# Performance work log

Measured on AMD Instinct MI355X. Metric: run time of the kernel, lower is better.

Reference implementation:

```python
import jax, jax.numpy as jnp
import numpy as np

N, E, C, Z, B, L = 50000, 800000, 32, 4, 8, 2
DEG = 16.0  # avg num neighbors = E / N


def ssp(x):
    # ShiftedSoftPlus
    return jax.nn.softplus(x) - jnp.log(2.0).astype(x.dtype)


def setup_inputs() -> dict:
    key = jax.random.key(0)
    ks = jax.random.split(key, 13)
    f32 = jnp.float32
    return {
        "node_features": jax.random.normal(ks[0], (N, 4 * C), f32),
        "node_attrs": jax.random.uniform(ks[1], (N, Z), f32),
        "edge_index": jax.random.randint(ks[2], (2, E), 0, N),
        "edge_embedding": jax.random.uniform(ks[3], (E, B), f32),
        "edge_attrs": jax.random.normal(ks[4], (E, 4), f32),
        "W0": jax.random.normal(ks[5], (L, C, C), f32) / np.sqrt(C),
        "W1": jax.random.normal(ks[6], (L, C, C), f32) / np.sqrt(C),
        "Wr1": jax.random.normal(ks[7], (L, B, B), f32) / np.sqrt(B),
        "Wr2": jax.random.normal(ks[8], (L, B, 5 * C), f32) / np.sqrt(B),
        "Ws": jax.random.normal(ks[9], (L, C, 2 * C), f32) / np.sqrt(C),
        "Wv": jax.random.normal(ks[10], (L, C, C), f32) / np.sqrt(C),
        "Wsc_s": jax.random.normal(ks[11], (L, C, Z, 2 * C), f32) / np.sqrt(C * Z),
        "Wsc_v": jax.random.normal(ks[12], (L, C, Z, C), f32) / np.sqrt(C * Z),
    }


def reference(node_features, node_attrs, edge_index, edge_embedding, edge_attrs,
              W0, W1, Wr1, Wr2, Ws, Wv, Wsc_s, Wsc_v):
    src, dst = edge_index[0], edge_index[1]
    Y0 = edge_attrs[:, :1]            # [E,1]  l=0 sph harmonic
    Yv = edge_attrs[:, 1:]            # [E,3]  l=1 sph harmonic
    x = node_features
    for l in range(L):
        s_in = x[:, :C]                          # [N,C]   scalars
        v_in = x[:, C:].reshape(N, C, 3)         # [N,C,3] vectors
        # linear (channel mixing per irrep)
        s = s_in @ W0[l]
        v = jnp.einsum('nci,cf->nfi', v_in, W1[l])
        # gather source node features per edge
        se = s[src]                              # [E,C]
        ve = v[src]                              # [E,C,3]
        # radial MLP -> per-edge tensor-product path weights (5 paths)
        w = jax.nn.silu(edge_embedding @ Wr1[l]) @ Wr2[l]   # [E,5C]
        w1, w2, w3, w4, w5 = jnp.split(w, 5, axis=-1)
        # tensor-product messages
        m_s = w1 * se * Y0 + w4 * jnp.einsum('eci,ei->ec', ve, Yv)          # 0ex0e->0e, 1ex1e->0e
        m_v = (w2[..., None] * se[..., None] * Yv[:, None, :]               # 0ex1e->1e
               + w3[..., None] * ve * Y0[..., None]                         # 1ex0e->1e
               + w5[..., None] * jnp.cross(ve, Yv[:, None, :]))             # 1ex1e->1e
        # scatter-sum to destination nodes, normalize by avg degree
        agg_s = jax.ops.segment_sum(m_s, dst, num_segments=N) / DEG
        agg_v = jax.ops.segment_sum(m_v, dst, num_segments=N) / DEG
        # output linear: scalars -> C feature scalars + C gates, vectors -> C
        out_s = agg_s @ Ws[l]                                               # [N,2C]
        out_v = jnp.einsum('nci,cf->nfi', agg_v, Wv[l])                     # [N,C,3]
        # self-connection (FullyConnectedTensorProduct with node_attrs)
        out_s = out_s + jnp.einsum('nc,nz,czf->nf', s_in, node_attrs, Wsc_s[l])
        out_v = out_v + jnp.einsum('nci,nz,czf->nfi', v_in, node_attrs, Wsc_v[l])
        # equivariant Gate nonlinearity
        feat = ssp(out_s[:, :C])
        gates = ssp(out_s[:, C:])
        gv = out_v * gates[..., None]
        new_x = jnp.concatenate([feat, gv.reshape(N, 3 * C)], axis=-1)
        x = x + new_x  # resnet (irreps match across layers)
    return x
```

## Files before the change

kernel.cpp:

```cpp
#include <hip/hip_runtime.h>
#include <math.h>

#define NN 50000
#define NE 800000
#define Cc 32
#define Zz 4
#define Bb 8
#define NL 2
#define DEG_INV (1.0f/16.0f)
#define SCAN_PAD 53248
#define EBLK (NE / 256)
#define NBLK (NN / 8)


__device__ __forceinline__ float ssp_f(float x) {
    float sp = fmaxf(x, 0.0f) + log1pf(expf(-fabsf(x)));
    return sp - 0.69314718055994530942f;
}
__device__ __forceinline__ float silu_f(float x) {
    return x / (1.0f + expf(-x));
}
__device__ __forceinline__ unsigned bf16rn(float f) {
    unsigned u = __float_as_uint(f);
    return (u + 0x7fffu + ((u >> 16) & 1u)) >> 16;
}


__global__ void hist_kernel(const int* __restrict__ ei, int* __restrict__ counts) {
    int e = blockIdx.x * 256 + threadIdx.x;
    if (e < NE) atomicAdd(&counts[ei[NE + e]], 1);
}

__global__ void scan_kernel(const int* __restrict__ counts,
                            int* __restrict__ base,
                            int* __restrict__ cursor) {
    __shared__ int partial[1024];
    int t = threadIdx.x;
    const int CH = 52;
    int b0 = t * CH;
    int sum = 0;
    #pragma unroll
    for (int i = 0; i < CH; i += 4) {
        int4 v = *(const int4*)(counts + b0 + i);
        sum += v.x + v.y + v.z + v.w;
    }
    partial[t] = sum;
    __syncthreads();
    for (int off = 1; off < 1024; off <<= 1) {
        int v = 0;
        if (t >= off) v = partial[t - off];
        __syncthreads();
        if (t >= off) partial[t] += v;
        __syncthreads();
    }
    int prefix = (t == 0) ? 0 : partial[t - 1];
    for (int i = b0; i < b0 + CH && i < NN; ++i) {
        base[i] = prefix;
        cursor[i] = prefix;
        prefix += counts[i];
    }
    if (t == 1023) base[NN] = partial[1023];
}

__global__ void prep_kernel(const int* __restrict__ ei,
                            const float* __restrict__ emb,
                            const float* __restrict__ eattr,
                            const float* __restrict__ Wr1,
                            int* __restrict__ cursor,
                            int* __restrict__ perm_src,
                            float* __restrict__ hS0,
                            float* __restrict__ hS1,
                            float* __restrict__ YS,
                            const float* __restrict__ nf,
                            const float* __restrict__ W0,
                            const float* __restrict__ W1,
                            float* __restrict__ x,
                            unsigned* __restrict__ svb) {
    __shared__ float wr1s[128];
    __shared__ float xs[8][128];
    int t = threadIdx.x;
    int b = blockIdx.x;
    if (b < EBLK) {
        if (t < 128) wr1s[t] = Wr1[t];
        __syncthreads();
        int e = b * 256 + t;
        int dst = ei[NE + e];
        int pos = atomicAdd(&cursor[dst], 1);
        perm_src[pos] = ei[e];

        const float4* s4 = (const float4*)emb + (size_t)e * 2;
        float4 a = s4[0], bb = s4[1];
        float em[8] = {a.x, a.y, a.z, a.w, bb.x, bb.y, bb.z, bb.w};
        float h0[8], h1[8];
        #pragma unroll
        for (int j = 0; j < 8; ++j) {
            float acc0 = 0.f, acc1 = 0.f;
            #pragma unroll
            for (int k = 0; k < 8; ++k) {
                acc0 = fmaf(em[k], wr1s[k * 8 + j], acc0);
                acc1 = fmaf(em[k], wr1s[64 + k * 8 + j], acc1);
            }
            h0[j] = silu_f(acc0);
            h1[j] = silu_f(acc1);
        }
        float4* o0 = (float4*)(hS0 + (size_t)pos * 8);
        o0[0] = make_float4(h0[0], h0[1], h0[2], h0[3]);
        o0[1] = make_float4(h0[4], h0[5], h0[6], h0[7]);
        float4* o1 = (float4*)(hS1 + (size_t)pos * 8);
        o1[0] = make_float4(h1[0], h1[1], h1[2], h1[3]);
        o1[1] = make_float4(h1[4], h1[5], h1[6], h1[7]);
        ((float4*)YS)[pos] = ((const float4*)eattr)[e];
    } else {
        int node0 = (b - EBLK) * 8;
        #pragma unroll
        for (int k = 0; k < 4; ++k) {
            int idx = t + k * 256;
            int n = idx >> 7, col = idx & 127;
            float val = nf[(size_t)(node0 + n) * 128 + col];
            xs[n][col] = val;
            x[(size_t)(node0 + n) * 128 + col] = val;
        }
        __syncthreads();
        int n = t >> 5, f = t & 31;
        int gn = node0 + n;
        float acc_s = 0.f, a0 = 0.f, a1 = 0.f, a2 = 0.f;
        #pragma unroll
        for (int c = 0; c < Cc; ++c) {
            float w0 = W0[c * Cc + f];
            float w1 = W1[c * Cc + f];
            acc_s = fmaf(xs[n][c], w0, acc_s);
            a0 = fmaf(xs[n][32 + c * 3 + 0], w1, a0);
            a1 = fmaf(xs[n][32 + c * 3 + 1], w1, a1);
            a2 = fmaf(xs[n][32 + c * 3 + 2], w1, a2);
        }
        unsigned* o = svb + (size_t)gn * 64;
        o[f]      = bf16rn(acc_s) | (bf16rn(a0) << 16);
        o[32 + f] = bf16rn(a1)    | (bf16rn(a2) << 16);
    }
}

#define PROC_EDGE(ha, hb, Yv, se, v0, v1, v2)                                \
    do {                                                                     \
        float hh0 = ha.x, hh1 = ha.y, hh2 = ha.z, hh3 = ha.w;                \
        float hh4 = hb.x, hh5 = hb.y, hh6 = hb.z, hh7 = hb.w;                \
        float w1 = 0.f, w2 = 0.f, w3 = 0.f, w4 = 0.f, w5 = 0.f;              \
        w1 = fmaf(hh0, wr2s[0][c], w1); w2 = fmaf(hh0, wr2s[0][32 + c], w2); \
        w3 = fmaf(hh0, wr2s[0][64 + c], w3); w4 = fmaf(hh0, wr2s[0][96 + c], w4); \
        w5 = fmaf(hh0, wr2s[0][128 + c], w5);                                \
        w1 = fmaf(hh1, wr2s[1][c], w1); w2 = fmaf(hh1, wr2s[1][32 + c], w2); \
        w3 = fmaf(hh1, wr2s[1][64 + c], w3); w4 = fmaf(hh1, wr2s[1][96 + c], w4); \
        w5 = fmaf(hh1, wr2s[1][128 + c], w5);                                \
        w1 = fmaf(hh2, wr2s[2][c], w1); w2 = fmaf(hh2, wr2s[2][32 + c], w2); \
        w3 = fmaf(hh2, wr2s[2][64 + c], w3); w4 = fmaf(hh2, wr2s[2][96 + c], w4); \
        w5 = fmaf(hh2, wr2s[2][128 + c], w5);                                \
        w1 = fmaf(hh3, wr2s[3][c], w1); w2 = fmaf(hh3, wr2s[3][32 + c], w2); \
        w3 = fmaf(hh3, wr2s[3][64 + c], w3); w4 = fmaf(hh3, wr2s[3][96 + c], w4); \
        w5 = fmaf(hh3, wr2s[3][128 + c], w5);                                \
        w1 = fmaf(hh4, wr2s[4][c], w1); w2 = fmaf(hh4, wr2s[4][32 + c], w2); \
        w3 = fmaf(hh4, wr2s[4][64 + c], w3); w4 = fmaf(hh4, wr2s[4][96 + c], w4); \
        w5 = fmaf(hh4, wr2s[4][128 + c], w5);                                \
        w1 = fmaf(hh5, wr2s[5][c], w1); w2 = fmaf(hh5, wr2s[5][32 + c], w2); \
        w3 = fmaf(hh5, wr2s[5][64 + c], w3); w4 = fmaf(hh5, wr2s[5][96 + c], w4); \
        w5 = fmaf(hh5, wr2s[5][128 + c], w5);                                \
        w1 = fmaf(hh6, wr2s[6][c], w1); w2 = fmaf(hh6, wr2s[6][32 + c], w2); \
        w3 = fmaf(hh6, wr2s[6][64 + c], w3); w4 = fmaf(hh6, wr2s[6][96 + c], w4); \
        w5 = fmaf(hh6, wr2s[6][128 + c], w5);                                \
        w1 = fmaf(hh7, wr2s[7][c], w1); w2 = fmaf(hh7, wr2s[7][32 + c], w2); \
        w3 = fmaf(hh7, wr2s[7][64 + c], w3); w4 = fmaf(hh7, wr2s[7][96 + c], w4); \
        w5 = fmaf(hh7, wr2s[7][128 + c], w5);                                \
        float dot = v0 * Yv.y + v1 * Yv.z + v2 * Yv.w;                       \
        ms += w1 * se * Yv.x + w4 * dot;                                     \
        float cx = v1 * Yv.w - v2 * Yv.z;                                    \
        float cy = v2 * Yv.y - v0 * Yv.w;                                    \
        float cz = v0 * Yv.z - v1 * Yv.y;                                    \
        mv0 += w2 * se * Yv.y + w3 * v0 * Yv.x + w5 * cx;                    \
        mv1 += w2 * se * Yv.z + w3 * v1 * Yv.x + w5 * cy;                    \
        mv2 += w2 * se * Yv.w + w3 * v2 * Yv.x + w5 * cz;                    \
    } while (0)

#define UNPACK_SV(p, se, v0, v1, v2)                                         \
    unsigned ulo_##se = (p)[c], uhi_##se = (p)[32 + c];                      \
    float se = __uint_as_float(ulo_##se << 16);                              \
    float v0 = __uint_as_float(ulo_##se & 0xffff0000u);                      \
    float v1 = __uint_as_float(uhi_##se << 16);                              \
    float v2 = __uint_as_float(uhi_##se & 0xffff0000u)

__global__ void agg_kernel(const int* __restrict__ base,
                           const int* __restrict__ perm_src,
                           const float* __restrict__ hS,
                           const float* __restrict__ YS,
                           const unsigned* __restrict__ svb,
                           const float* __restrict__ Wr2,
                           float* __restrict__ agg) {
    __shared__ float wr2s[8][160];
    int t = threadIdx.x;
    for (int i = t; i < 8 * 160; i += 256) ((float*)wr2s)[i] = Wr2[i];
    __syncthreads();
    int n = blockIdx.x * 8 + (t >> 5);
    int c = t & 31;
    int jb = base[n], je = base[n + 1];
    float ms = 0.f, mv0 = 0.f, mv1 = 0.f, mv2 = 0.f;

    for (int j0 = jb; j0 < je; j0 += 32) {
        int myidx = j0 + c;
        int src_l = (myidx < je) ? perm_src[myidx] : 0;
        int cnt = min(32, je - j0);
        int i = 0;
        for (; i + 1 < cnt; i += 2) {
            int srcA = __shfl(src_l, i, 32);
            int srcB = __shfl(src_l, i + 1, 32);
            const unsigned* pA = svb + (size_t)srcA * 64;
            const unsigned* pB = svb + (size_t)srcB * 64;
            UNPACK_SV(pA, seA, vA0, vA1, vA2);
            UNPACK_SV(pB, seB, vB0, vB1, vB2);
            const float4* hA4 = (const float4*)(hS + (size_t)(j0 + i) * 8);
            float4 hAa = hA4[0], hAb = hA4[1];
            float4 YA = ((const float4*)YS)[j0 + i];
            const float4* hB4 = (const float4*)(hS + (size_t)(j0 + i + 1) * 8);
            float4 hBa = hB4[0], hBb = hB4[1];
            float4 YB = ((const float4*)YS)[j0 + i + 1];
            PROC_EDGE(hAa, hAb, YA, seA, vA0, vA1, vA2);
            PROC_EDGE(hBa, hBb, YB, seB, vB0, vB1, vB2);
        }
        if (i < cnt) {
            int srcA = __shfl(src_l, i, 32);
            const unsigned* pA = svb + (size_t)srcA * 64;
            UNPACK_SV(pA, seA, vA0, vA1, vA2);
            const float4* hA4 = (const float4*)(hS + (size_t)(j0 + i) * 8);
            float4 hAa = hA4[0], hAb = hA4[1];
            float4 YA = ((const float4*)YS)[j0 + i];
            PROC_EDGE(hAa, hAb, YA, seA, vA0, vA1, vA2);
        }
    }

    float* ap = agg + (size_t)n * 128;
    ap[c]      = ms * DEG_INV;
    ap[32 + c] = mv0 * DEG_INV;
    ap[64 + c] = mv1 * DEG_INV;
    ap[96 + c] = mv2 * DEG_INV;
}

template <int WANT_SV>
__global__ void post_pre_kernel(float* __restrict__ x,
                                const float* __restrict__ attrs,
                                const float* __restrict__ agg,
                                const float* __restrict__ Ws,
                                const float* __restrict__ Wv,
                                const float* __restrict__ Wsc_s,
                                const float* __restrict__ Wsc_v,
                                const float* __restrict__ W0n,
                                const float* __restrict__ W1n,
                                unsigned* __restrict__ svb) {
    __shared__ float shx[32][128];
    __shared__ float sha[32][128];
    int t = threadIdx.x;
    int node0 = blockIdx.x * 32;
    #pragma unroll
    for (int k = 0; k < 4; ++k) {
        int f4 = t + k * 256;
        int n = f4 >> 5, col4 = f4 & 31;
        int gn = node0 + n;
        if (gn < NN) {
            ((float4*)&shx[n][0])[col4] = ((const float4*)(x + (size_t)gn * 128))[col4];
            ((float4*)&sha[n][0])[col4] = ((const float4*)(agg + (size_t)gn * 128))[col4];
        }
    }
    __syncthreads();
    int g = t >> 5, f = t & 31;

    float az[4][4];
    #pragma unroll
    for (int k = 0; k < 4; ++k) {
        int gn = node0 + g + k * 8;
        if (gn < NN) {
            float4 a4 = ((const float4*)attrs)[gn];
            az[k][0] = a4.x; az[k][1] = a4.y; az[k][2] = a4.z; az[k][3] = a4.w;
        } else {
            az[k][0] = az[k][1] = az[k][2] = az[k][3] = 0.f;
        }
    }

    float os0[4] = {0, 0, 0, 0}, os1[4] = {0, 0, 0, 0};
    float ov0[4] = {0, 0, 0, 0}, ov1[4] = {0, 0, 0, 0}, ov2[4] = {0, 0, 0, 0};

    #pragma unroll 2
    for (int c = 0; c < Cc; ++c) {
        float ws0 = Ws[c * 64 + f];
        float ws1 = Ws[c * 64 + 32 + f];
        float wv  = Wv[c * 32 + f];
        #pragma unroll
        for (int k = 0; k < 4; ++k) {
            int n = g + k * 8;
            float as  = sha[n][c];
            float av0 = sha[n][32 + c];
            float av1 = sha[n][64 + c];
            float av2 = sha[n][96 + c];
            os0[k] = fmaf(as, ws0, os0[k]);
            os1[k] = fmaf(as, ws1, os1[k]);
            ov0[k] = fmaf(av0, wv, ov0[k]);
            ov1[k] = fmaf(av1, wv, ov1[k]);
            ov2[k] = fmaf(av2, wv, ov2[k]);
        }
        #pragma unroll
        for (int z = 0; z < 4; ++z) {
            int cz = c * 4 + z;
            float wss0 = Wsc_s[cz * 64 + f];
            float wss1 = Wsc_s[cz * 64 + 32 + f];
            float wsv  = Wsc_v[cz * 32 + f];
            #pragma unroll
            for (int k = 0; k < 4; ++k) {
                int n = g + k * 8;
                float azv = az[k][z];
                float sa = shx[n][c] * azv;
                os0[k] = fmaf(sa, wss0, os0[k]);
                os1[k] = fmaf(sa, wss1, os1[k]);
                float va = azv * wsv;
                ov0[k] = fmaf(shx[n][32 + c * 3 + 0], va, ov0[k]);
                ov1[k] = fmaf(shx[n][32 + c * 3 + 1], va, ov1[k]);
                ov2[k] = fmaf(shx[n][32 + c * 3 + 2], va, ov2[k]);
            }
        }
    }

    float ns[4], nv0[4], nv1[4], nv2[4];
    #pragma unroll
    for (int k = 0; k < 4; ++k) {
        int n = g + k * 8;
        int gn = node0 + n;
        float feat = ssp_f(os0[k]);
        float gate = ssp_f(os1[k]);
        ns[k]  = shx[n][f] + feat;
        nv0[k] = shx[n][32 + f * 3 + 0] + ov0[k] * gate;
        nv1[k] = shx[n][32 + f * 3 + 1] + ov1[k] * gate;
        nv2[k] = shx[n][32 + f * 3 + 2] + ov2[k] * gate;
        if (gn < NN) {
            float* xp = x + (size_t)gn * 128;
            xp[f] = ns[k];
            xp[32 + f * 3 + 0] = nv0[k];
            xp[32 + f * 3 + 1] = nv1[k];
            xp[32 + f * 3 + 2] = nv2[k];
        }
    }

    if (WANT_SV) {
        __syncthreads();
        #pragma unroll
        for (int k = 0; k < 4; ++k) {
            int n = g + k * 8;
            sha[n][f] = ns[k];
            sha[n][32 + f * 3 + 0] = nv0[k];
            sha[n][32 + f * 3 + 1] = nv1[k];
            sha[n][32 + f * 3 + 2] = nv2[k];
        }
        __syncthreads();
        float bs[4] = {0, 0, 0, 0};
        float b0[4] = {0, 0, 0, 0}, b1[4] = {0, 0, 0, 0}, b2[4] = {0, 0, 0, 0};
        #pragma unroll 4
        for (int c = 0; c < Cc; ++c) {
            float w0 = W0n[c * Cc + f];
            float w1 = W1n[c * Cc + f];
            #pragma unroll
            for (int k = 0; k < 4; ++k) {
                int n = g + k * 8;
                bs[k] = fmaf(sha[n][c], w0, bs[k]);
                b0[k] = fmaf(sha[n][32 + c * 3 + 0], w1, b0[k]);
                b1[k] = fmaf(sha[n][32 + c * 3 + 1], w1, b1[k]);
                b2[k] = fmaf(sha[n][32 + c * 3 + 2], w1, b2[k]);
            }
        }
        #pragma unroll
        for (int k = 0; k < 4; ++k) {
            int gn = node0 + g + k * 8;
            if (gn < NN) {
                unsigned* o = svb + (size_t)gn * 64;
                o[f]      = bf16rn(bs[k]) | (bf16rn(b0[k]) << 16);
                o[32 + f] = bf16rn(b1[k]) | (bf16rn(b2[k]) << 16);
            }
        }
    }
}

__global__ void edge_atomic_kernel(const int* __restrict__ ei,
                                   const float* __restrict__ emb,
                                   const float* __restrict__ eattr,
                                   const unsigned* __restrict__ svb,
                                   const float* __restrict__ Wr1,
                                   const float* __restrict__ Wr2,
                                   float* __restrict__ agg) {
    int t = threadIdx.x;
    int eg = t >> 5;
    int c = t & 31;
    int e = blockIdx.x * 8 + eg;
    if (e >= NE) return;
    int src = ei[e];
    int dst = ei[NE + e];
    float h = 0.f;
    if (c < 8) {
        #pragma unroll
        for (int k = 0; k < 8; ++k)
            h = fmaf(emb[e * 8 + k], Wr1[k * 8 + c], h);
        h = silu_f(h);
    }
    float w1 = 0.f, w2 = 0.f, w3 = 0.f, w4 = 0.f, w5 = 0.f;
    #pragma unroll
    for (int j = 0; j < 8; ++j) {
        float hj = __shfl(h, j, 32);
        const float* wr = Wr2 + j * 160;
        w1 = fmaf(hj, wr[c], w1);
        w2 = fmaf(hj, wr[32 + c], w2);
        w3 = fmaf(hj, wr[64 + c], w3);
        w4 = fmaf(hj, wr[96 + c], w4);
        w5 = fmaf(hj, wr[128 + c], w5);
    }
    float Y0  = eattr[e * 4 + 0];
    float Yv0 = eattr[e * 4 + 1];
    float Yv1 = eattr[e * 4 + 2];
    float Yv2 = eattr[e * 4 + 3];
    const unsigned* p = svb + (size_t)src * 64;
    unsigned ulo = p[c], uhi = p[32 + c];
    float se  = __uint_as_float(ulo << 16);
    float ve0 = __uint_as_float(ulo & 0xffff0000u);
    float ve1 = __uint_as_float(uhi << 16);
    float ve2 = __uint_as_float(uhi & 0xffff0000u);
    float dot = ve0 * Yv0 + ve1 * Yv1 + ve2 * Yv2;
    float msg = (w1 * se * Y0 + w4 * dot) * DEG_INV;
    float cx = ve1 * Yv2 - ve2 * Yv1;
    float cy = ve2 * Yv0 - ve0 * Yv2;
    float cz = ve0 * Yv1 - ve1 * Yv0;
    float mv0 = (w2 * se * Yv0 + w3 * ve0 * Y0 + w5 * cx) * DEG_INV;
    float mv1 = (w2 * se * Yv1 + w3 * ve1 * Y0 + w5 * cy) * DEG_INV;
    float mv2 = (w2 * se * Yv2 + w3 * ve2 * Y0 + w5 * cz) * DEG_INV;
    float* ap = agg + (size_t)dst * 128;
    atomicAdd(&ap[c], msg);
    atomicAdd(&ap[32 + c], mv0);
    atomicAdd(&ap[64 + c], mv1);
    atomicAdd(&ap[96 + c], mv2);
}

__global__ void init_kernel(const float* __restrict__ nf,
                            const float* __restrict__ W0,
                            const float* __restrict__ W1,
                            float* __restrict__ x,
                            unsigned* __restrict__ svb) {
    __shared__ float xs[8][128];
    int t = threadIdx.x;
    int node0 = blockIdx.x * 8;
    #pragma unroll
    for (int k = 0; k < 4; ++k) {
        int idx = t + k * 256;
        int n = idx >> 7, col = idx & 127;
        float val = nf[(size_t)(node0 + n) * 128 + col];
        xs[n][col] = val;
        x[(size_t)(node0 + n) * 128 + col] = val;
    }
    __syncthreads();
    int n = t >> 5, f = t & 31;
    int gn = node0 + n;
    float acc_s = 0.f, a0 = 0.f, a1 = 0.f, a2 = 0.f;
    #pragma unroll
    for (int c = 0; c < Cc; ++c) {
        float w0 = W0[c * Cc + f];
        float w1 = W1[c * Cc + f];
        acc_s = fmaf(xs[n][c], w0, acc_s);
        a0 = fmaf(xs[n][32 + c * 3 + 0], w1, a0);
        a1 = fmaf(xs[n][32 + c * 3 + 1], w1, a1);
        a2 = fmaf(xs[n][32 + c * 3 + 2], w1, a2);
    }
    unsigned* o = svb + (size_t)gn * 64;
    o[f]      = bf16rn(acc_s) | (bf16rn(a0) << 16);
    o[32 + f] = bf16rn(a1)    | (bf16rn(a2) << 16);
}

extern "C" void kernel_launch(void* const* d_in, const int* in_sizes, int n_in,
                              void* d_out, int out_size, void* d_ws, size_t ws_size,
                              hipStream_t stream) {
    const float* node_features  = (const float*)d_in[0];
    const float* node_attrs     = (const float*)d_in[1];
    const int*   edge_index     = (const int*)d_in[2];
    const float* edge_embedding = (const float*)d_in[3];
    const float* edge_attrs     = (const float*)d_in[4];
    const float* W0    = (const float*)d_in[5];
    const float* W1    = (const float*)d_in[6];
    const float* Wr1   = (const float*)d_in[7];
    const float* Wr2   = (const float*)d_in[8];
    const float* Ws    = (const float*)d_in[9];
    const float* Wv    = (const float*)d_in[10];
    const float* Wsc_s = (const float*)d_in[11];
    const float* Wsc_v = (const float*)d_in[12];

    float* x = (float*)d_out;

    float* ws = (float*)d_ws;
    unsigned* svb = (unsigned*)ws;
    float* agg  = (float*)(svb + (size_t)NN * 64);
    float* hS0  = agg + (size_t)NN * 128;
    float* hS1  = hS0 + (size_t)NE * 8;
    float* YS   = hS1 + (size_t)NE * 8;
    int* counts   = (int*)(YS + (size_t)NE * 4);
    int* base     = counts + SCAN_PAD;
    int* cursor   = base + NN + 1;
    int* perm_src = cursor + NN;
    size_t needed = ((char*)(perm_src + NE)) - (char*)d_ws;

    bool use_sorted = ws_size >= needed;
    const int PP_GRID = (NN + 31) / 32;

    if (use_sorted) {
        hipMemsetAsync(counts, 0, SCAN_PAD * sizeof(int), stream);
        hist_kernel<<<NE / 256, 256, 0, stream>>>(edge_index, counts);
        scan_kernel<<<1, 1024, 0, stream>>>(counts, base, cursor);
        prep_kernel<<<EBLK + NBLK, 256, 0, stream>>>(
            edge_index, edge_embedding, edge_attrs, Wr1,
            cursor, perm_src, hS0, hS1, YS,
            node_features, W0, W1, x, svb);

        agg_kernel<<<NN / 8, 256, 0, stream>>>(base, perm_src, hS0, YS, svb,
                                               Wr2, agg);
        post_pre_kernel<1><<<PP_GRID, 256, 0, stream>>>(
            x, node_attrs, agg, Ws, Wv, Wsc_s, Wsc_v,
            W0 + Cc * Cc, W1 + Cc * Cc, svb);
        agg_kernel<<<NN / 8, 256, 0, stream>>>(base, perm_src, hS1, YS, svb,
                                               Wr2 + Bb * 5 * Cc, agg);
        post_pre_kernel<0><<<PP_GRID, 256, 0, stream>>>(
            x, node_attrs, agg,
            Ws + Cc * 2 * Cc, Wv + Cc * Cc,
            Wsc_s + Cc * Zz * 2 * Cc, Wsc_v + Cc * Zz * Cc,
            nullptr, nullptr, nullptr);
    } else {
        hipMemcpyAsync(x, node_features, (size_t)NN * 128 * sizeof(float),
                       hipMemcpyDeviceToDevice, stream);
        for (int l = 0; l < NL; ++l) {
            hipMemsetAsync(agg, 0, (size_t)NN * 128 * sizeof(float), stream);
            init_kernel<<<NN / 8, 256, 0, stream>>>(
                x, W0 + l * Cc * Cc, W1 + l * Cc * Cc, x, svb);
            edge_atomic_kernel<<<NE / 8, 256, 0, stream>>>(
                edge_index, edge_embedding, edge_attrs, svb,
                Wr1 + l * Bb * Bb, Wr2 + l * Bb * 5 * Cc, agg);
            post_pre_kernel<0><<<PP_GRID, 256, 0, stream>>>(
                x, node_attrs, agg,
                Ws + l * Cc * 2 * Cc, Wv + l * Cc * Cc,
                Wsc_s + l * Cc * Zz * 2 * Cc, Wsc_v + l * Cc * Zz * Cc,
                nullptr, nullptr, nullptr);
        }
    }
}
```

Before: 536.0 us.

## Pack per-edge radial hidden, attrs and src into one 64-byte record

Per-edge data that used to sit in separate arrays (two fp32 radial hidden vectors, the edge attributes, the permuted src index) is now stored in one 64-byte record holding bf16 hidden vectors for both layers, the fp32 attrs and the src index. The aggregation kernel reads one contiguous record per edge and no longer loads src indices in 32-wide chunks and broadcasts them with shuffles. This cuts per-edge write and read traffic and gives coalesced record loads. In exchange the radial hidden activations lose precision through bf16 rounding, and each lane now loads src directly, which puts a dependent load ahead of the svb gather.

Result: no change. 541.0 us (+0.9%).

```diff
diff --git a/kernel.cpp b/kernel.cpp
--- a/kernel.cpp
+++ b/kernel.cpp
@@ -67,10 +67,7 @@
                             const float* __restrict__ eattr,
                             const float* __restrict__ Wr1,
                             int* __restrict__ cursor,
-                            int* __restrict__ perm_src,
-                            float* __restrict__ hS0,
-                            float* __restrict__ hS1,
-                            float* __restrict__ YS,
+                            uint4* __restrict__ rec,
                             const float* __restrict__ nf,
                             const float* __restrict__ W0,
                             const float* __restrict__ W1,
@@ -84,9 +81,9 @@
         if (t < 128) wr1s[t] = Wr1[t];
         __syncthreads();
         int e = b * 256 + t;
+        int src = ei[e];
         int dst = ei[NE + e];
         int pos = atomicAdd(&cursor[dst], 1);
-        perm_src[pos] = ei[e];
 
         const float4* s4 = (const float4*)emb + (size_t)e * 2;
         float4 a = s4[0], bb = s4[1];
@@ -103,13 +100,20 @@
             h0[j] = silu_f(acc0);
             h1[j] = silu_f(acc1);
         }
-        float4* o0 = (float4*)(hS0 + (size_t)pos * 8);
-        o0[0] = make_float4(h0[0], h0[1], h0[2], h0[3]);
-        o0[1] = make_float4(h0[4], h0[5], h0[6], h0[7]);
-        float4* o1 = (float4*)(hS1 + (size_t)pos * 8);
-        o1[0] = make_float4(h1[0], h1[1], h1[2], h1[3]);
-        o1[1] = make_float4(h1[4], h1[5], h1[6], h1[7]);
-        ((float4*)YS)[pos] = ((const float4*)eattr)[e];
+        uint4 u0, u1;
+        u0.x = bf16rn(h0[0]) | (bf16rn(h0[1]) << 16);
+        u0.y = bf16rn(h0[2]) | (bf16rn(h0[3]) << 16);
+        u0.z = bf16rn(h0[4]) | (bf16rn(h0[5]) << 16);
+        u0.w = bf16rn(h0[6]) | (bf16rn(h0[7]) << 16);
+        u1.x = bf16rn(h1[0]) | (bf16rn(h1[1]) << 16);
+        u1.y = bf16rn(h1[2]) | (bf16rn(h1[3]) << 16);
+        u1.z = bf16rn(h1[4]) | (bf16rn(h1[5]) << 16);
+        u1.w = bf16rn(h1[6]) | (bf16rn(h1[7]) << 16);
+        uint4* r = rec + (size_t)pos * 4;
+        r[0] = u0;
+        r[1] = u1;
+        r[2] = ((const uint4*)eattr)[e];
+        r[3] = make_uint4((unsigned)src, 0u, 0u, 0u);
     } else {
         int node0 = (b - EBLK) * 8;
         #pragma unroll
@@ -139,10 +143,16 @@
     }
 }
 
-#define PROC_EDGE(ha, hb, Yv, se, v0, v1, v2)                                \
+#define PROC_EDGE_PK(ua, Yv, se, v0, v1, v2)                                 \
     do {                                                                     \
-        float hh0 = ha.x, hh1 = ha.y, hh2 = ha.z, hh3 = ha.w;                \
-        float hh4 = hb.x, hh5 = hb.y, hh6 = hb.z, hh7 = hb.w;                \
+        float hh0 = __uint_as_float(ua.x << 16);                             \
+        float hh1 = __uint_as_float(ua.x & 0xffff0000u);                     \
+        float hh2 = __uint_as_float(ua.y << 16);                             \
+        float hh3 = __uint_as_float(ua.y & 0xffff0000u);                     \
+        float hh4 = __uint_as_float(ua.z << 16);                             \
+        float hh5 = __uint_as_float(ua.z & 0xffff0000u);                     \
+        float hh6 = __uint_as_float(ua.w << 16);                             \
+        float hh7 = __uint_as_float(ua.w & 0xffff0000u);                     \
         float w1 = 0.f, w2 = 0.f, w3 = 0.f, w4 = 0.f, w5 = 0.f;              \
         w1 = fmaf(hh0, wr2s[0][c], w1); w2 = fmaf(hh0, wr2s[0][32 + c], w2); \
         w3 = fmaf(hh0, wr2s[0][64 + c], w3); w4 = fmaf(hh0, wr2s[0][96 + c], w4); \
@@ -186,9 +196,8 @@
     float v2 = __uint_as_float(uhi_##se & 0xffff0000u)
 
 __global__ void agg_kernel(const int* __restrict__ base,
-                           const int* __restrict__ perm_src,
-                           const float* __restrict__ hS,
-                           const float* __restrict__ YS,
+                           const uint4* __restrict__ rec,
+                           const int lsel,
                            const unsigned* __restrict__ svb,
                            const float* __restrict__ Wr2,
                            float* __restrict__ agg) {
@@ -201,36 +210,31 @@
     int jb = base[n], je = base[n + 1];
     float ms = 0.f, mv0 = 0.f, mv1 = 0.f, mv2 = 0.f;
 
-    for (int j0 = jb; j0 < je; j0 += 32) {
-        int myidx = j0 + c;
-        int src_l = (myidx < je) ? perm_src[myidx] : 0;
-        int cnt = min(32, je - j0);
-        int i = 0;
-        for (; i + 1 < cnt; i += 2) {
-            int srcA = __shfl(src_l, i, 32);
-            int srcB = __shfl(src_l, i + 1, 32);
-            const unsigned* pA = svb + (size_t)srcA * 64;
-            const unsigned* pB = svb + (size_t)srcB * 64;
-            UNPACK_SV(pA, seA, vA0, vA1, vA2);
-            UNPACK_SV(pB, seB, vB0, vB1, vB2);
-            const float4* hA4 = (const float4*)(hS + (size_t)(j0 + i) * 8);
-            float4 hAa = hA4[0], hAb = hA4[1];
-            float4 YA = ((const float4*)YS)[j0 + i];
-            const float4* hB4 = (const float4*)(hS + (size_t)(j0 + i + 1) * 8);
-            float4 hBa = hB4[0], hBb = hB4[1];
-            float4 YB = ((const float4*)YS)[j0 + i + 1];
-            PROC_EDGE(hAa, hAb, YA, seA, vA0, vA1, vA2);
-            PROC_EDGE(hBa, hBb, YB, seB, vB0, vB1, vB2);
-        }
-        if (i < cnt) {
-            int srcA = __shfl(src_l, i, 32);
-            const unsigned* pA = svb + (size_t)srcA * 64;
-            UNPACK_SV(pA, seA, vA0, vA1, vA2);
-            const float4* hA4 = (const float4*)(hS + (size_t)(j0 + i) * 8);
-            float4 hAa = hA4[0], hAb = hA4[1];
-            float4 YA = ((const float4*)YS)[j0 + i];
-            PROC_EDGE(hAa, hAb, YA, seA, vA0, vA1, vA2);
-        }
+    int j = jb;
+    for (; j + 1 < je; j += 2) {
+        const uint4* rA = rec + (size_t)j * 4;
+        const uint4* rB = rA + 4;
+        uint4 uA = rA[lsel];
+        float4 YA = *(const float4*)(rA + 2);
+        int srcA = (int)rA[3].x;
+        uint4 uB = rB[lsel];
+        float4 YB = *(const float4*)(rB + 2);
+        int srcB = (int)rB[3].x;
+        const unsigned* pA = svb + (size_t)srcA * 64;
+        const unsigned* pB = svb + (size_t)srcB * 64;
+        UNPACK_SV(pA, seA, vA0, vA1, vA2);
+        UNPACK_SV(pB, seB, vB0, vB1, vB2);
+        PROC_EDGE_PK(uA, YA, seA, vA0, vA1, vA2);
+        PROC_EDGE_PK(uB, YB, seB, vB0, vB1, vB2);
+    }
+    if (j < je) {
+        const uint4* rA = rec + (size_t)j * 4;
+        uint4 uA = rA[lsel];
+        float4 YA = *(const float4*)(rA + 2);
+        int srcA = (int)rA[3].x;
+        const unsigned* pA = svb + (size_t)srcA * 64;
+        UNPACK_SV(pA, seA, vA0, vA1, vA2);
+        PROC_EDGE_PK(uA, YA, seA, vA0, vA1, vA2);
     }
 
     float* ap = agg + (size_t)n * 128;
@@ -493,14 +497,11 @@
     float* ws = (float*)d_ws;
     unsigned* svb = (unsigned*)ws;
     float* agg  = (float*)(svb + (size_t)NN * 64);
-    float* hS0  = agg + (size_t)NN * 128;
-    float* hS1  = hS0 + (size_t)NE * 8;
-    float* YS   = hS1 + (size_t)NE * 8;
-    int* counts   = (int*)(YS + (size_t)NE * 4);
+    uint4* rec  = (uint4*)(agg + (size_t)NN * 128);
+    int* counts   = (int*)(rec + (size_t)NE * 4);
     int* base     = counts + SCAN_PAD;
     int* cursor   = base + NN + 1;
-    int* perm_src = cursor + NN;
-    size_t needed = ((char*)(perm_src + NE)) - (char*)d_ws;
+    size_t needed = ((char*)(cursor + NN)) - (char*)d_ws;
 
     bool use_sorted = ws_size >= needed;
     const int PP_GRID = (NN + 31) / 32;
@@ -511,15 +512,14 @@
         scan_kernel<<<1, 1024, 0, stream>>>(counts, base, cursor);
         prep_kernel<<<EBLK + NBLK, 256, 0, stream>>>(
             edge_index, edge_embedding, edge_attrs, Wr1,
-            cursor, perm_src, hS0, hS1, YS,
+            cursor, rec,
             node_features, W0, W1, x, svb);
 
-        agg_kernel<<<NN / 8, 256, 0, stream>>>(base, perm_src, hS0, YS, svb,
-                                               Wr2, agg);
+        agg_kernel<<<NN / 8, 256, 0, stream>>>(base, rec, 0, svb, Wr2, agg);
         post_pre_kernel<1><<<PP_GRID, 256, 0, stream>>>(
             x, node_attrs, agg, Ws, Wv, Wsc_s, Wsc_v,
             W0 + Cc * Cc, W1 + Cc * Cc, svb);
-        agg_kernel<<<NN / 8, 256, 0, stream>>>(base, perm_src, hS1, YS, svb,
+        agg_kernel<<<NN / 8, 256, 0, stream>>>(base, rec, 1, svb,
                                                Wr2 + Bb * 5 * Cc, agg);
         post_pre_kernel<0><<<PP_GRID, 256, 0, stream>>>(
             x, node_attrs, agg,
```
